# Kernel optimization log

Hardware: AMD Instinct MI355X
Metric: run time of the kernel (lower is better)

The kernel has to match this reference:

```python
import jax, jax.numpy as jnp
import numpy as np

N_PATHS = 200000
PATH_LEN = 8
N_LINKS = 20000
MAX_PL = 100  # max paths crossing a link
DIM = 16
ITERS = 8
# min-max normalization constants: (min, scale) as in set_min_max_scores
MM_TRAFFIC = (0.0, 1e-4)
MM_PACKETS = (0.0, 1e-2)
MM_PKTSIZE = (0.0, 1e-3)
MM_CAP = (0.0, 1e-1)


def _gru(x, h, k, rk, b):
    # Keras GRUCell, reset_after=True. b: [2, 3*units] (input bias, recurrent bias)
    mx = x @ k + b[0]
    mi = h @ rk + b[1]
    xz, xr, xh = jnp.split(mx, 3, axis=-1)
    rz, rr, rh = jnp.split(mi, 3, axis=-1)
    z = jax.nn.sigmoid(xz + rz)
    r = jax.nn.sigmoid(xr + rr)
    hh = jnp.tanh(xh + r * rh)
    return z * h + (1.0 - z) * hh


def setup_inputs() -> dict:
    key = jax.random.key(0)
    ks = jax.random.split(key, 24)
    f32 = jnp.float32
    inp = {}
    inp['flow_traffic'] = jax.random.uniform(ks[0], (N_PATHS, 1), f32, 100.0, 10000.0)
    inp['flow_packets'] = jax.random.uniform(ks[1], (N_PATHS, 1), f32, 1.0, 100.0)
    inp['flow_packet_size'] = jax.random.uniform(ks[2], (N_PATHS, 1), f32, 100.0, 1500.0)
    inp['flow_type'] = jax.random.uniform(ks[3], (N_PATHS, 2), f32)
    inp['link_capacity'] = jax.random.uniform(ks[4], (N_LINKS, 1), f32, 10.0, 100.0)
    inp['link_to_path'] = jax.random.randint(ks[5], (N_PATHS, PATH_LEN), 0, N_LINKS, jnp.int32)
    p_idx = jax.random.randint(ks[6], (N_LINKS, MAX_PL), 0, N_PATHS, jnp.int32)
    s_idx = jax.random.randint(ks[7], (N_LINKS, MAX_PL), 0, PATH_LEN + 1, jnp.int32)
    inp['path_to_link'] = jnp.stack([p_idx, s_idx], axis=-1)

    def dense(k, i, o):
        return jax.random.normal(k, (i, o), f32) * (1.0 / np.sqrt(i))

    inp['fe_w1'] = dense(ks[8], 5, DIM);   inp['fe_b1'] = jnp.zeros((DIM,), f32)
    inp['fe_w2'] = dense(ks[9], DIM, DIM); inp['fe_b2'] = jnp.zeros((DIM,), f32)
    inp['le_w1'] = dense(ks[10], 2, DIM);  inp['le_b1'] = jnp.zeros((DIM,), f32)
    inp['le_w2'] = dense(ks[11], DIM, DIM); inp['le_b2'] = jnp.zeros((DIM,), f32)
    inp['pgru_k'] = dense(ks[12], DIM, 3 * DIM)
    inp['pgru_rk'] = dense(ks[13], DIM, 3 * DIM)
    inp['pgru_b'] = jnp.zeros((2, 3 * DIM), f32)
    inp['lgru_k'] = dense(ks[14], DIM, 3 * DIM)
    inp['lgru_rk'] = dense(ks[15], DIM, 3 * DIM)
    inp['lgru_b'] = jnp.zeros((2, 3 * DIM), f32)
    inp['ro_w1'] = dense(ks[16], DIM, DIM // 2); inp['ro_b1'] = jnp.zeros((DIM // 2,), f32)
    inp['ro_w2'] = dense(ks[17], DIM // 2, DIM // 4); inp['ro_b2'] = jnp.zeros((DIM // 4,), f32)
    inp['ro_w3'] = dense(ks[18], DIM // 4, 1); inp['ro_b3'] = jnp.zeros((1,), f32)
    return inp


def reference(flow_traffic, flow_packets, flow_packet_size, flow_type, link_capacity,
              link_to_path, path_to_link,
              fe_w1, fe_b1, fe_w2, fe_b2, le_w1, le_b1, le_w2, le_b2,
              pgru_k, pgru_rk, pgru_b, lgru_k, lgru_rk, lgru_b,
              ro_w1, ro_b1, ro_w2, ro_b2, ro_w3, ro_b3):
    relu = jax.nn.relu
    # load per link: sum traffic of crossing paths / capacity
    load = jnp.sum(flow_traffic[path_to_link[:, :, 0]], axis=1) / (link_capacity * 1e9)  # [L,1]

    flow_feats = jnp.concatenate([
        (flow_traffic - MM_TRAFFIC[0]) * MM_TRAFFIC[1],
        (flow_packets - MM_PACKETS[0]) * MM_PACKETS[1],
        (flow_packet_size - MM_PKTSIZE[0]) * MM_PKTSIZE[1],
        flow_type], axis=1)  # [P,5]
    path_state = relu(relu(flow_feats @ fe_w1 + fe_b1) @ fe_w2 + fe_b2)  # [P,16]

    link_feats = jnp.concatenate([(link_capacity - MM_CAP[0]) * MM_CAP[1], load], axis=1)  # [L,2]
    link_state = relu(relu(link_feats @ le_w1 + le_b1) @ le_w2 + le_b2)  # [L,16]

    for _ in range(ITERS):
        link_gather = link_state[link_to_path]  # [P, path_len, 16]
        prev = path_state

        def step(h, x):
            h2 = _gru(x, h, pgru_k, pgru_rk, pgru_b)
            return h2, h2

        path_state, seq = jax.lax.scan(step, prev, jnp.swapaxes(link_gather, 0, 1))
        seq = jnp.swapaxes(seq, 0, 1)  # [P, path_len, 16]
        path_state_sequence = jnp.concatenate([prev[:, None, :], seq], axis=1)  # [P, path_len+1, 16]
        # gather_nd: (path_idx, seq_pos) pairs per link
        path_gather = path_state_sequence[path_to_link[:, :, 0], path_to_link[:, :, 1]]  # [L, MAX_PL, 16]
        path_sum = jnp.sum(path_gather, axis=1)  # [L,16]
        link_state = _gru(path_sum, link_state, lgru_k, lgru_rk, lgru_b)

    h1 = relu(path_state_sequence[:, 1:] @ ro_w1 + ro_b1)
    h2 = relu(h1 @ ro_w2 + ro_b2)
    occupancy = jax.nn.softplus(h2 @ ro_w3 + ro_b3)  # [P, path_len, 1]
    capacity_gather = link_capacity[link_to_path]  # [P, path_len, 1]
    delay = jnp.sum(occupancy / capacity_gather, axis=1)  # [P,1]
    return delay
```

## Files before the change

### kernel.cpp

```cpp
#include <hip/hip_runtime.h>
#include <hip/hip_bf16.h>
#include <math.h>

#define N_PATHS  200000
#define PATH_LEN 8
#define N_LINKS  20000
#define MAX_PL   100
#define DIM      16
#define ITERS    8

typedef __attribute__((ext_vector_type(8))) short bf16x8;
typedef __attribute__((ext_vector_type(4))) float f32x4;

#define SEQ_BYTES  64000000ull
#define LS_BYTES   1280000ull
#define LREC_BYTES 1280000ull
#define P2L_BYTES  8000000ull
#define SLOT_BYTES 6400000u

__device__ __forceinline__ float fast_sigmoid(float x) {
    return __builtin_amdgcn_rcpf(1.0f + __expf(-x));
}
__device__ __forceinline__ float fast_tanh(float x) {
    float ax = fabsf(x);
    float t  = __expf(-2.0f * ax);
    float r  = (1.0f - t) * __builtin_amdgcn_rcpf(1.0f + t);
    return copysignf(r, x);
}
__device__ __forceinline__ float softplusf_(float x) {
    return fmaxf(x, 0.0f) + log1pf(expf(-fabsf(x)));
}
__device__ __forceinline__ float bflo(unsigned int u) {
    union { unsigned int i; float f; } c; c.i = u << 16; return c.f;
}
__device__ __forceinline__ float bfhi(unsigned int u) {
    union { unsigned int i; float f; } c; c.i = u & 0xffff0000u; return c.f;
}
__device__ __forceinline__ unsigned int pk_bf16(float lo, float hi) {
    unsigned int r;
    asm("v_cvt_pk_bf16_f32 %0, %1, %2" : "=v"(r) : "v"(lo), "v"(hi));
    return r;
}
__device__ __forceinline__ unsigned short bf16_1(float v) {
    return (unsigned short)(pk_bf16(v, v) & 0xffffu);
}

union U8 { unsigned int u[4]; bf16x8 v; };

__global__ __launch_bounds__(256) void k_pack(const int* __restrict__ p2l,
                                              unsigned int* __restrict__ outE,
                                              unsigned int* __restrict__ outO)
{
    int i = blockIdx.x * 256 + threadIdx.x;
    if (i < N_LINKS * MAX_PL) {
        unsigned int pi = (unsigned int)p2l[2 * i];
        unsigned int si = (unsigned int)p2l[2 * i + 1];
        unsigned int sE = (si == 0) ? 8u : ((si == 8) ? 9u : si);
        unsigned int sO = (si == 0) ? 9u : ((si == 8) ? 8u : si);
        outE[i] = (sE << 18) | pi;
        outO[i] = (sO << 18) | pi;
    }
}

__global__ __launch_bounds__(64) void k_init_links(
    const float* __restrict__ traffic, const float* __restrict__ cap,
    const int* __restrict__ p2l,
    const float* __restrict__ le_w1, const float* __restrict__ le_b1,
    const float* __restrict__ le_w2, const float* __restrict__ le_b2,
    const float* __restrict__ kk, const float* __restrict__ pb,
    float* __restrict__ ls, unsigned short* __restrict__ lrec)
{
    int l = blockIdx.x;
    int lane = threadIdx.x;
    float s = 0.0f;
    for (int j = lane; j < MAX_PL; j += 64) {
        int p = p2l[(size_t)(l * MAX_PL + j) * 2 + 0];
        s += traffic[p];
    }
    #pragma unroll
    for (int off = 32; off > 0; off >>= 1) s += __shfl_xor(s, off);

    float c = cap[l];
    float f0 = c * 0.1f;
    float f1 = s / (c * 1e9f);

    float h1[DIM];
    #pragma unroll
    for (int d = 0; d < DIM; d++)
        h1[d] = fmaxf(f0 * le_w1[d] + f1 * le_w1[DIM + d] + le_b1[d], 0.0f);

    float h2[DIM];
    #pragma unroll
    for (int d = 0; d < DIM; d++) {
        float a = le_b2[d];
        #pragma unroll
        for (int k = 0; k < DIM; k++) a = fmaf(h1[k], le_w2[k * DIM + d], a);
        h2[d] = fmaxf(a, 0.0f);
    }
    if (lane < DIM) ls[(size_t)l * DIM + lane] = h2[lane];
    if (lane < DIM) {
        float mh = pb[32 + lane];
        #pragma unroll
        for (int k = 0; k < DIM; k++) mh = fmaf(h2[k], kk[k * 48 + 32 + lane], mh);
        unsigned short* rec = lrec + (size_t)l * 32;
        int q = lane >> 2, idx = lane & 3;
        rec[q * 8 + idx]     = bf16_1(h2[lane]);
        rec[q * 8 + 4 + idx] = bf16_1(mh);
    }
}

__global__ __launch_bounds__(256) void k_init_paths(
    const float* __restrict__ traffic, const float* __restrict__ packets,
    const float* __restrict__ pktsize, const float* __restrict__ ftype,
    const float* __restrict__ fe_w1, const float* __restrict__ fe_b1,
    const float* __restrict__ fe_w2, const float* __restrict__ fe_b2,
    unsigned short* __restrict__ seq)
{
    int p = blockIdx.x * blockDim.x + threadIdx.x;
    if (p >= N_PATHS) return;
    float f[5];
    f[0] = traffic[p] * 0.0001f;
    f[1] = packets[p] * 0.01f;
    f[2] = pktsize[p] * 0.001f;
    f[3] = ftype[p * 2 + 0];
    f[4] = ftype[p * 2 + 1];

    float h1[DIM];
    #pragma unroll
    for (int d = 0; d < DIM; d++) {
        float a = fe_b1[d];
        #pragma unroll
        for (int k = 0; k < 5; k++) a = fmaf(f[k], fe_w1[k * DIM + d], a);
        h1[d] = fmaxf(a, 0.0f);
    }
    float h2[DIM];
    #pragma unroll
    for (int d = 0; d < DIM; d++) {
        float a = fe_b2[d];
        #pragma unroll
        for (int k = 0; k < DIM; k++) a = fmaf(h1[k], fe_w2[k * DIM + d], a);
        h2[d] = fmaxf(a, 0.0f);
    }
    unsigned int pkd[8];
    #pragma unroll
    for (int q = 0; q < 8; q++) pkd[q] = pk_bf16(h2[2 * q], h2[2 * q + 1]);
    uint4* out = (uint4*)(seq + ((size_t)8 * N_PATHS + p) * DIM);
    out[0] = make_uint4(pkd[0], pkd[1], pkd[2], pkd[3]);
    out[1] = make_uint4(pkd[4], pkd[5], pkd[6], pkd[7]);
}

__global__ __launch_bounds__(256, 4) void k_paths(
    const int* __restrict__ l2p, const unsigned short* __restrict__ lrec,
    const float* __restrict__ rk, const float* __restrict__ kk,
    const float* __restrict__ b,
    unsigned short* __restrict__ seq, int ps, int cs)
{
    int l = threadIdx.x & 63;
    int wave = (blockIdx.x * 256 + threadIdx.x) >> 6;
    int pr = l & 15;
    int g  = l >> 4;
    int kq = g * 4;
    int p  = wave * 16 + pr;

    U8 Az, Ar, Ah;
    {
        #pragma unroll
        for (int i = 0; i < 2; i++) {
            int k0 = (kq + 2 * i) * 48, k1 = (kq + 2 * i + 1) * 48;
            Az.u[i]     = pk_bf16(rk[k0 + pr],      rk[k1 + pr]);
            Az.u[2 + i] = pk_bf16(kk[k0 + pr],      kk[k1 + pr]);
            Ar.u[i]     = pk_bf16(rk[k0 + 16 + pr], rk[k1 + 16 + pr]);
            Ar.u[2 + i] = pk_bf16(kk[k0 + 16 + pr], kk[k1 + 16 + pr]);
            Ah.u[i]     = pk_bf16(rk[k0 + 32 + pr], rk[k1 + 32 + pr]);
            Ah.u[2 + i] = 0;
        }
    }
    f32x4 Cz, Cr, Ch;
    #pragma unroll
    for (int r = 0; r < 4; r++) {
        Cz[r] = b[kq + r]      + b[48 + kq + r];
        Cr[r] = b[16 + kq + r] + b[64 + kq + r];
        Ch[r] = b[80 + kq + r];
    }

    int4 ia = *(const int4*)(l2p + (size_t)p * 8);
    int4 ib = *(const int4*)(l2p + (size_t)p * 8 + 4);
#define IDX(t) ((t) == 0 ? ia.x : (t) == 1 ? ia.y : (t) == 2 ? ia.z : (t) == 3 ? ia.w : \
                (t) == 4 ? ib.x : (t) == 5 ? ib.y : (t) == 6 ? ib.z : ib.w)

    const char* lrecc = (const char*)lrec;
    char* seqc = (char*)seq;
    unsigned g16 = (unsigned)(g * 16);
    unsigned sbase = (unsigned)p * 32u + (unsigned)(g * 8);
    unsigned csoff = (unsigned)cs * SLOT_BYTES + sbase;

    uint4 X[8];
    #pragma unroll
    for (int t = 0; t < 8; t++)
        X[t] = *(const uint4*)(lrecc + (unsigned)IDX(t) * 64u + g16);

    float h0, h1, h2, h3;
    U8 B;
    {
        uint2 hp = *(const uint2*)(seqc + ((unsigned)ps * SLOT_BYTES + sbase));
        h0 = bflo(hp.x); h1 = bfhi(hp.x); h2 = bflo(hp.y); h3 = bfhi(hp.y);
        B.u[0] = hp.x; B.u[1] = hp.y;
    }

#define STEPX(t, soff) { \
    B.u[2] = X[t].x; B.u[3] = X[t].y; \
    f32x4 az = __builtin_amdgcn_mfma_f32_16x16x32_bf16(Az.v, B.v, Cz, 0, 0, 0); \
    f32x4 ar = __builtin_amdgcn_mfma_f32_16x16x32_bf16(Ar.v, B.v, Cr, 0, 0, 0); \
    f32x4 ah = __builtin_amdgcn_mfma_f32_16x16x32_bf16(Ah.v, B.v, Ch, 0, 0, 0); \
    float z0 = fast_sigmoid(az[0]), z1 = fast_sigmoid(az[1]); \
    float z2 = fast_sigmoid(az[2]), z3 = fast_sigmoid(az[3]); \
    float r0 = fast_sigmoid(ar[0]), r1 = fast_sigmoid(ar[1]); \
    float r2 = fast_sigmoid(ar[2]), r3 = fast_sigmoid(ar[3]); \
    float q0 = fast_tanh(bflo(X[t].z) + r0 * ah[0]); \
    float q1 = fast_tanh(bfhi(X[t].z) + r1 * ah[1]); \
    float q2 = fast_tanh(bflo(X[t].w) + r2 * ah[2]); \
    float q3 = fast_tanh(bfhi(X[t].w) + r3 * ah[3]); \
    h0 = z0 * h0 + (1.0f - z0) * q0; \
    h1 = z1 * h1 + (1.0f - z1) * q1; \
    h2 = z2 * h2 + (1.0f - z2) * q2; \
    h3 = z3 * h3 + (1.0f - z3) * q3; \
    unsigned int p01 = pk_bf16(h0, h1), p23 = pk_bf16(h2, h3); \
    *(uint2*)(seqc + (soff)) = make_uint2(p01, p23); \
    B.u[0] = p01; B.u[1] = p23; }

    STEPX(0, 1u * SLOT_BYTES + sbase)
    STEPX(1, 2u * SLOT_BYTES + sbase)
    STEPX(2, 3u * SLOT_BYTES + sbase)
    STEPX(3, 4u * SLOT_BYTES + sbase)
    STEPX(4, 5u * SLOT_BYTES + sbase)
    STEPX(5, 6u * SLOT_BYTES + sbase)
    STEPX(6, 7u * SLOT_BYTES + sbase)
    STEPX(7, csoff)
#undef STEPX
#undef IDX
}

__global__ __launch_bounds__(256) void k_links(
    const unsigned int* __restrict__ p2lp, const unsigned short* __restrict__ seq,
    const float* __restrict__ lk, const float* __restrict__ lrk,
    const float* __restrict__ lb,
    const float* __restrict__ kk, const float* __restrict__ pb,
    float* ls, unsigned short* __restrict__ lrec)
{
    int lane = threadIdx.x & 63;
    int l = blockIdx.x * 4 + (threadIdx.x >> 6);
    size_t base = (size_t)l * MAX_PL;
    int half = lane & 1;
    int r0 = lane >> 1;

    unsigned int e0 = p2lp[base + r0];
    unsigned int e1 = p2lp[base + r0 + 32];
    unsigned int e2 = p2lp[base + r0 + 64];

    const unsigned short* sh = seq + half * 8;
    unsigned int pi, si;
    pi = e0 & 0x3FFFFu; si = e0 >> 18;
    uint4 a0 = *(const uint4*)(sh + ((size_t)si * N_PATHS + pi) * DIM);
    pi = e1 & 0x3FFFFu; si = e1 >> 18;
    uint4 a1 = *(const uint4*)(sh + ((size_t)si * N_PATHS + pi) * DIM);
    pi = e2 & 0x3FFFFu; si = e2 >> 18;
    uint4 a2 = *(const uint4*)(sh + ((size_t)si * N_PATHS + pi) * DIM);

    float acc[8];
    #pragma unroll
    for (int i = 0; i < 8; i++) acc[i] = 0.0f;
    unsigned int selLo = 0x00003F80u;
    unsigned int selHi = 0x3F800000u;

#define DOTU(u, i0) \
    asm("v_dot2_f32_bf16 %0, %1, %2, %0" : "+v"(acc[i0]) : "v"(u), "v"(selLo)); \
    asm("v_dot2_f32_bf16 %0, %1, %2, %0" : "+v"(acc[i0 + 1]) : "v"(u), "v"(selHi));
#define DOT8(a) DOTU(a.x, 0) DOTU(a.y, 2) DOTU(a.z, 4) DOTU(a.w, 6)

    DOT8(a0) DOT8(a1) DOT8(a2)
    if (r0 < 4) {
        unsigned int e3 = p2lp[base + r0 + 96];
        pi = e3 & 0x3FFFFu; si = e3 >> 18;
        uint4 a3 = *(const uint4*)(sh + ((size_t)si * N_PATHS + pi) * DIM);
        DOT8(a3)
    }
#undef DOTU
#undef DOT8

    float v4[4];
    {
        int sel = (lane & 2) ? 4 : 0;
        #pragma unroll
        for (int i = 0; i < 4; i++)
            v4[i] = acc[sel + i] + __shfl_xor(acc[(4 - sel) + i], 2);
    }
    float v2[2];
    {
        int sel = (lane & 4) ? 2 : 0;
        #pragma unroll
        for (int i = 0; i < 2; i++)
            v2[i] = v4[sel + i] + __shfl_xor(v4[(2 - sel) + i], 4);
    }
    float s;
    {
        int sel = (lane & 8) ? 1 : 0;
        s = v2[sel] + __shfl_xor(v2[1 - sel], 8);
    }
    s += __shfl_xor(s, 16);
    s += __shfl_xor(s, 32);

    float accf[16];
    #pragma unroll
    for (int k = 0; k < 16; k++) {
        int src = ((k >> 3) & 1) | (((k >> 2) & 1) << 1) | (((k >> 1) & 1) << 2) | ((k & 1) << 3);
        accf[k] = __shfl(s, src);
    }

    float h[DIM];
    #pragma unroll
    for (int d = 0; d < DIM; d++) h[d] = ls[(size_t)l * DIM + d];

    int j = (lane < 48) ? lane : 0;
    float mx = lb[j];
    float mi = lb[48 + j];
    #pragma unroll
    for (int k = 0; k < DIM; k++) {
        mx = fmaf(accf[k], lk[k * 48 + j], mx);
        mi = fmaf(h[k],   lrk[k * 48 + j], mi);
    }

    int d = lane & 15;
    float xz = __shfl(mx, d),      rz = __shfl(mi, d);
    float xr = __shfl(mx, d + 16), rr = __shfl(mi, d + 16);
    float xh = __shfl(mx, d + 32), rh = __shfl(mi, d + 32);
    float z  = fast_sigmoid(xz + rz);
    float r  = fast_sigmoid(xr + rr);
    float hh = fast_tanh(xh + r * rh);
    float hn = z * h[d] + (1.0f - z) * hh;

    if (lane < DIM) ls[(size_t)l * DIM + lane] = hn;

    float hf[DIM];
    #pragma unroll
    for (int k = 0; k < DIM; k++) hf[k] = __shfl(hn, k);
    if (lane < DIM) {
        float mh = pb[32 + lane];
        #pragma unroll
        for (int k = 0; k < DIM; k++) mh = fmaf(hf[k], kk[k * 48 + 32 + lane], mh);
        unsigned short* rec = lrec + (size_t)l * 32;
        int q = lane >> 2, idx = lane & 3;
        rec[q * 8 + idx]     = bf16_1(hn);
        rec[q * 8 + 4 + idx] = bf16_1(mh);
    }
}

__global__ __launch_bounds__(256) void k_readout(
    const unsigned short* __restrict__ seq, const int* __restrict__ l2p,
    const float* __restrict__ cap,
    const float* __restrict__ w1, const float* __restrict__ b1,
    const float* __restrict__ w2, const float* __restrict__ b2,
    const float* __restrict__ w3, const float* __restrict__ b3,
    float* __restrict__ out)
{
    int p = blockIdx.x * blockDim.x + threadIdx.x;
    if (p >= N_PATHS) return;
    float delay = 0.0f;
    for (int t = 1; t <= PATH_LEN; t++) {
        const uint4* gp = (const uint4*)(seq + ((size_t)t * N_PATHS + p) * DIM);
        uint4 a = gp[0], c = gp[1];
        float h[DIM];
        h[0]  = bflo(a.x); h[1]  = bfhi(a.x); h[2]  = bflo(a.y); h[3]  = bfhi(a.y);
        h[4]  = bflo(a.z); h[5]  = bfhi(a.z); h[6]  = bflo(a.w); h[7]  = bfhi(a.w);
        h[8]  = bflo(c.x); h[9]  = bfhi(c.x); h[10] = bflo(c.y); h[11] = bfhi(c.y);
        h[12] = bflo(c.z); h[13] = bfhi(c.z); h[14] = bflo(c.w); h[15] = bfhi(c.w);

        float h1[8];
        #pragma unroll
        for (int jj = 0; jj < 8; jj++) {
            float a1 = b1[jj];
            #pragma unroll
            for (int k = 0; k < DIM; k++) a1 = fmaf(h[k], w1[k * 8 + jj], a1);
            h1[jj] = fmaxf(a1, 0.0f);
        }
        float h2[4];
        #pragma unroll
        for (int jj = 0; jj < 4; jj++) {
            float a2 = b2[jj];
            #pragma unroll
            for (int k = 0; k < 8; k++) a2 = fmaf(h1[k], w2[k * 4 + jj], a2);
            h2[jj] = fmaxf(a2, 0.0f);
        }
        float o = b3[0];
        #pragma unroll
        for (int k = 0; k < 4; k++) o = fmaf(h2[k], w3[k], o);
        o = softplusf_(o);

        float cp = cap[l2p[(size_t)p * PATH_LEN + (t - 1)]];
        delay += o / cp;
    }
    out[p] = delay;
}

extern "C" void kernel_launch(void* const* d_in, const int* in_sizes, int n_in,
                              void* d_out, int out_size, void* d_ws, size_t ws_size,
                              hipStream_t stream)
{
    const float* flow_traffic = (const float*)d_in[0];
    const float* flow_packets = (const float*)d_in[1];
    const float* flow_pktsize = (const float*)d_in[2];
    const float* flow_type    = (const float*)d_in[3];
    const float* link_cap     = (const float*)d_in[4];
    const int*   l2p          = (const int*)d_in[5];
    const int*   p2l          = (const int*)d_in[6];
    const float* fe_w1 = (const float*)d_in[7];
    const float* fe_b1 = (const float*)d_in[8];
    const float* fe_w2 = (const float*)d_in[9];
    const float* fe_b2 = (const float*)d_in[10];
    const float* le_w1 = (const float*)d_in[11];
    const float* le_b1 = (const float*)d_in[12];
    const float* le_w2 = (const float*)d_in[13];
    const float* le_b2 = (const float*)d_in[14];
    const float* pgru_k  = (const float*)d_in[15];
    const float* pgru_rk = (const float*)d_in[16];
    const float* pgru_b  = (const float*)d_in[17];
    const float* lgru_k  = (const float*)d_in[18];
    const float* lgru_rk = (const float*)d_in[19];
    const float* lgru_b  = (const float*)d_in[20];
    const float* ro_w1 = (const float*)d_in[21];
    const float* ro_b1 = (const float*)d_in[22];
    const float* ro_w2 = (const float*)d_in[23];
    const float* ro_b2 = (const float*)d_in[24];
    const float* ro_w3 = (const float*)d_in[25];
    const float* ro_b3 = (const float*)d_in[26];
    float* out = (float*)d_out;

    char* ws = (char*)d_ws;
    unsigned short* seq   = (unsigned short*)ws;
    float*          ls    = (float*)(ws + SEQ_BYTES);
    unsigned short* lrec  = (unsigned short*)(ws + SEQ_BYTES + LS_BYTES);
    unsigned int*   p2lpE = (unsigned int*)(ws + SEQ_BYTES + LS_BYTES + LREC_BYTES);
    unsigned int*   p2lpO = (unsigned int*)(ws + SEQ_BYTES + LS_BYTES + LREC_BYTES + P2L_BYTES);

    k_pack<<<(N_LINKS * MAX_PL + 255) / 256, 256, 0, stream>>>(p2l, p2lpE, p2lpO);
    k_init_links<<<N_LINKS, 64, 0, stream>>>(flow_traffic, link_cap, p2l,
        le_w1, le_b1, le_w2, le_b2, pgru_k, pgru_b, ls, lrec);
    k_init_paths<<<(N_PATHS + 255) / 256, 256, 0, stream>>>(flow_traffic,
        flow_packets, flow_pktsize, flow_type, fe_w1, fe_b1, fe_w2, fe_b2, seq);

    for (int it = 0; it < ITERS; ++it) {
        int ps = (it & 1) ? 9 : 8;
        int cs = (it & 1) ? 8 : 9;
        k_paths<<<(N_PATHS / 16) / 4, 256, 0, stream>>>(l2p, lrec, pgru_rk,
            pgru_k, pgru_b, seq, ps, cs);
        if (it != ITERS - 1)
            k_links<<<N_LINKS / 4, 256, 0, stream>>>((it & 1) ? p2lpO : p2lpE,
                seq, lgru_k, lgru_rk, lgru_b, pgru_k, pgru_b, ls, lrec);
    }

    k_readout<<<(N_PATHS + 255) / 256, 256, 0, stream>>>(seq, l2p, link_cap,
        ro_w1, ro_b1, ro_w2, ro_b2, ro_w3, ro_b3, out);
}
```

Before: 561.2 us.

## Fuse readout MLP into final path GRU pass and drop separate readout kernel

The last path-GRU iteration becomes a dedicated kernel that runs the readout MLP right after each step. The first layer uses an MFMA and the rest runs in registers with a cross-lane shuffle, so the final sequence states are never written to or re-read from global memory. Softplus switches to hardware exp2/log approximations, and the occupancy hint on k_paths is dropped. This removes one kernel launch and the readout's pass over the sequence buffer, at the cost of more registers in the fused kernel and a bf16 first readout layer.

```diff
diff --git a/kernel.cpp b/kernel.cpp
--- a/kernel.cpp
+++ b/kernel.cpp
@@ -27,8 +27,10 @@
     float r  = (1.0f - t) * __builtin_amdgcn_rcpf(1.0f + t);
     return copysignf(r, x);
 }
-__device__ __forceinline__ float softplusf_(float x) {
-    return fmaxf(x, 0.0f) + log1pf(expf(-fabsf(x)));
+__device__ __forceinline__ float fast_softplus(float x) {
+    float e = __builtin_amdgcn_exp2f(-fabsf(x) * 1.44269504f);
+    float lg = __builtin_amdgcn_logf(1.0f + e);
+    return fmaxf(x, 0.0f) + 0.69314718f * lg;
 }
 __device__ __forceinline__ float bflo(unsigned int u) {
     union { unsigned int i; float f; } c; c.i = u << 16; return c.f;
@@ -149,7 +151,7 @@
     out[1] = make_uint4(pkd[4], pkd[5], pkd[6], pkd[7]);
 }
 
-__global__ __launch_bounds__(256, 4) void k_paths(
+__global__ __launch_bounds__(256) void k_paths(
     const int* __restrict__ l2p, const unsigned short* __restrict__ lrec,
     const float* __restrict__ rk, const float* __restrict__ kk,
     const float* __restrict__ b,
@@ -237,7 +239,136 @@
     STEPX(6, 7u * SLOT_BYTES + sbase)
     STEPX(7, csoff)
 #undef STEPX
+}
+
+__global__ __launch_bounds__(256) void k_paths_last(
+    const int* __restrict__ l2p, const unsigned short* __restrict__ lrec,
+    const float* __restrict__ rk, const float* __restrict__ kk,
+    const float* __restrict__ b,
+    const unsigned short* __restrict__ seq,
+    const float* __restrict__ cap,
+    const float* __restrict__ w1, const float* __restrict__ b1,
+    const float* __restrict__ w2, const float* __restrict__ b2,
+    const float* __restrict__ w3, const float* __restrict__ b3,
+    float* __restrict__ out, int ps)
+{
+    int l = threadIdx.x & 63;
+    int wave = (blockIdx.x * 256 + threadIdx.x) >> 6;
+    int pr = l & 15;
+    int g  = l >> 4;
+    int kq = g * 4;
+    int p  = wave * 16 + pr;
+
+    U8 Az, Ar, Ah, A1;
+    {
+        #pragma unroll
+        for (int i = 0; i < 2; i++) {
+            int k0 = (kq + 2 * i) * 48, k1 = (kq + 2 * i + 1) * 48;
+            Az.u[i]     = pk_bf16(rk[k0 + pr],      rk[k1 + pr]);
+            Az.u[2 + i] = pk_bf16(kk[k0 + pr],      kk[k1 + pr]);
+            Ar.u[i]     = pk_bf16(rk[k0 + 16 + pr], rk[k1 + 16 + pr]);
+            Ar.u[2 + i] = pk_bf16(kk[k0 + 16 + pr], kk[k1 + 16 + pr]);
+            Ah.u[i]     = pk_bf16(rk[k0 + 32 + pr], rk[k1 + 32 + pr]);
+            Ah.u[2 + i] = 0;
+            A1.u[i]     = (pr < 8) ? pk_bf16(w1[(kq + 2 * i) * 8 + pr],
+                                             w1[(kq + 2 * i + 1) * 8 + pr]) : 0u;
+            A1.u[2 + i] = 0;
+        }
+    }
+    f32x4 Cz, Cr, Ch, C1;
+    #pragma unroll
+    for (int r = 0; r < 4; r++) {
+        Cz[r] = b[kq + r]      + b[48 + kq + r];
+        Cr[r] = b[16 + kq + r] + b[64 + kq + r];
+        Ch[r] = b[80 + kq + r];
+        C1[r] = (kq + r < 8) ? b1[kq + r] : 0.0f;
+    }
+    float W2[8][4], B2v[4], W3[4], B3v;
+    #pragma unroll
+    for (int k = 0; k < 8; k++)
+        #pragma unroll
+        for (int j = 0; j < 4; j++) W2[k][j] = w2[k * 4 + j];
+    #pragma unroll
+    for (int j = 0; j < 4; j++) B2v[j] = b2[j];
+    #pragma unroll
+    for (int j = 0; j < 4; j++) W3[j] = w3[j];
+    B3v = b3[0];
+
+    int4 ia = *(const int4*)(l2p + (size_t)p * 8);
+    int4 ib = *(const int4*)(l2p + (size_t)p * 8 + 4);
+
+    const char* lrecc = (const char*)lrec;
+    const char* seqc = (const char*)seq;
+    unsigned g16 = (unsigned)(g * 16);
+    unsigned sbase = (unsigned)p * 32u + (unsigned)(g * 8);
+
+    uint4 X[8];
+    float capv[8];
+    #pragma unroll
+    for (int t = 0; t < 8; t++) {
+        int li = IDX(t);
+        X[t] = *(const uint4*)(lrecc + (unsigned)li * 64u + g16);
+        capv[t] = cap[li];
+    }
+
+    float h0, h1, h2, h3;
+    U8 B;
+    {
+        uint2 hp = *(const uint2*)(seqc + ((unsigned)ps * SLOT_BYTES + sbase));
+        h0 = bflo(hp.x); h1 = bfhi(hp.x); h2 = bflo(hp.y); h3 = bfhi(hp.y);
+        B.u[0] = hp.x; B.u[1] = hp.y;
+    }
+    U8 Bro;
+    Bro.u[2] = 0; Bro.u[3] = 0;
+    float delay = 0.0f;
+
+#define STEPL(t) { \
+    B.u[2] = X[t].x; B.u[3] = X[t].y; \
+    f32x4 az = __builtin_amdgcn_mfma_f32_16x16x32_bf16(Az.v, B.v, Cz, 0, 0, 0); \
+    f32x4 ar = __builtin_amdgcn_mfma_f32_16x16x32_bf16(Ar.v, B.v, Cr, 0, 0, 0); \
+    f32x4 ah = __builtin_amdgcn_mfma_f32_16x16x32_bf16(Ah.v, B.v, Ch, 0, 0, 0); \
+    float z0 = fast_sigmoid(az[0]), z1 = fast_sigmoid(az[1]); \
+    float z2 = fast_sigmoid(az[2]), z3 = fast_sigmoid(az[3]); \
+    float r0 = fast_sigmoid(ar[0]), r1 = fast_sigmoid(ar[1]); \
+    float r2 = fast_sigmoid(ar[2]), r3 = fast_sigmoid(ar[3]); \
+    float q0 = fast_tanh(bflo(X[t].z) + r0 * ah[0]); \
+    float q1 = fast_tanh(bfhi(X[t].z) + r1 * ah[1]); \
+    float q2 = fast_tanh(bflo(X[t].w) + r2 * ah[2]); \
+    float q3 = fast_tanh(bfhi(X[t].w) + r3 * ah[3]); \
+    h0 = z0 * h0 + (1.0f - z0) * q0; \
+    h1 = z1 * h1 + (1.0f - z1) * q1; \
+    h2 = z2 * h2 + (1.0f - z2) * q2; \
+    h3 = z3 * h3 + (1.0f - z3) * q3; \
+    unsigned int p01 = pk_bf16(h0, h1), p23 = pk_bf16(h2, h3); \
+    B.u[0] = p01; B.u[1] = p23; \
+    Bro.u[0] = p01; Bro.u[1] = p23; \
+    f32x4 d1 = __builtin_amdgcn_mfma_f32_16x16x32_bf16(A1.v, Bro.v, C1, 0, 0, 0); \
+    float e0 = fmaxf(d1[0], 0.0f), e1 = fmaxf(d1[1], 0.0f); \
+    float e2 = fmaxf(d1[2], 0.0f), e3 = fmaxf(d1[3], 0.0f); \
+    float f0 = __shfl_xor(e0, 16), f1 = __shfl_xor(e1, 16); \
+    float f2 = __shfl_xor(e2, 16), f3 = __shfl_xor(e3, 16); \
+    float hh2[4]; \
+    _Pragma("unroll") \
+    for (int j = 0; j < 4; j++) { \
+        float a2 = B2v[j]; \
+        a2 = fmaf(e0, W2[0][j], a2); a2 = fmaf(e1, W2[1][j], a2); \
+        a2 = fmaf(e2, W2[2][j], a2); a2 = fmaf(e3, W2[3][j], a2); \
+        a2 = fmaf(f0, W2[4][j], a2); a2 = fmaf(f1, W2[5][j], a2); \
+        a2 = fmaf(f2, W2[6][j], a2); a2 = fmaf(f3, W2[7][j], a2); \
+        hh2[j] = fmaxf(a2, 0.0f); \
+    } \
+    float o = B3v; \
+    o = fmaf(hh2[0], W3[0], o); o = fmaf(hh2[1], W3[1], o); \
+    o = fmaf(hh2[2], W3[2], o); o = fmaf(hh2[3], W3[3], o); \
+    o = fast_softplus(o); \
+    delay += o * __builtin_amdgcn_rcpf(capv[t]); }
+
+    STEPL(0) STEPL(1) STEPL(2) STEPL(3)
+    STEPL(4) STEPL(5) STEPL(6) STEPL(7)
+#undef STEPL
 #undef IDX
+
+    if (g == 0) out[p] = delay;
 }
 
 __global__ __launch_bounds__(256) void k_links(
@@ -352,53 +483,6 @@
         rec[q * 8 + idx]     = bf16_1(hn);
         rec[q * 8 + 4 + idx] = bf16_1(mh);
     }
-}
-
-__global__ __launch_bounds__(256) void k_readout(
-    const unsigned short* __restrict__ seq, const int* __restrict__ l2p,
-    const float* __restrict__ cap,
-    const float* __restrict__ w1, const float* __restrict__ b1,
-    const float* __restrict__ w2, const float* __restrict__ b2,
-    const float* __restrict__ w3, const float* __restrict__ b3,
-    float* __restrict__ out)
-{
-    int p = blockIdx.x * blockDim.x + threadIdx.x;
-    if (p >= N_PATHS) return;
-    float delay = 0.0f;
-    for (int t = 1; t <= PATH_LEN; t++) {
-        const uint4* gp = (const uint4*)(seq + ((size_t)t * N_PATHS + p) * DIM);
-        uint4 a = gp[0], c = gp[1];
-        float h[DIM];
-        h[0]  = bflo(a.x); h[1]  = bfhi(a.x); h[2]  = bflo(a.y); h[3]  = bfhi(a.y);
-        h[4]  = bflo(a.z); h[5]  = bfhi(a.z); h[6]  = bflo(a.w); h[7]  = bfhi(a.w);
-        h[8]  = bflo(c.x); h[9]  = bfhi(c.x); h[10] = bflo(c.y); h[11] = bfhi(c.y);
-        h[12] = bflo(c.z); h[13] = bfhi(c.z); h[14] = bflo(c.w); h[15] = bfhi(c.w);
-
-        float h1[8];
-        #pragma unroll
-        for (int jj = 0; jj < 8; jj++) {
-            float a1 = b1[jj];
-            #pragma unroll
-            for (int k = 0; k < DIM; k++) a1 = fmaf(h[k], w1[k * 8 + jj], a1);
-            h1[jj] = fmaxf(a1, 0.0f);
-        }
-        float h2[4];
-        #pragma unroll
-        for (int jj = 0; jj < 4; jj++) {
-            float a2 = b2[jj];
-            #pragma unroll
-            for (int k = 0; k < 8; k++) a2 = fmaf(h1[k], w2[k * 4 + jj], a2);
-            h2[jj] = fmaxf(a2, 0.0f);
-        }
-        float o = b3[0];
-        #pragma unroll
-        for (int k = 0; k < 4; k++) o = fmaf(h2[k], w3[k], o);
-        o = softplusf_(o);
-
-        float cp = cap[l2p[(size_t)p * PATH_LEN + (t - 1)]];
-        delay += o / cp;
-    }
-    out[p] = delay;
 }
 
 extern "C" void kernel_launch(void* const* d_in, const int* in_sizes, int n_in,
@@ -447,16 +531,15 @@
     k_init_paths<<<(N_PATHS + 255) / 256, 256, 0, stream>>>(flow_traffic,
         flow_packets, flow_pktsize, flow_type, fe_w1, fe_b1, fe_w2, fe_b2, seq);
 
-    for (int it = 0; it < ITERS; ++it) {
+    for (int it = 0; it < ITERS - 1; ++it) {
         int ps = (it & 1) ? 9 : 8;
         int cs = (it & 1) ? 8 : 9;
         k_paths<<<(N_PATHS / 16) / 4, 256, 0, stream>>>(l2p, lrec, pgru_rk,
             pgru_k, pgru_b, seq, ps, cs);
-        if (it != ITERS - 1)
-            k_links<<<N_LINKS / 4, 256, 0, stream>>>((it & 1) ? p2lpO : p2lpE,
-                seq, lgru_k, lgru_rk, lgru_b, pgru_k, pgru_b, ls, lrec);
-    }
-
-    k_readout<<<(N_PATHS + 255) / 256, 256, 0, stream>>>(seq, l2p, link_cap,
-        ro_w1, ro_b1, ro_w2, ro_b2, ro_w3, ro_b3, out);
-}
+        k_links<<<N_LINKS / 4, 256, 0, stream>>>((it & 1) ? p2lpO : p2lpE,
+            seq, lgru_k, lgru_rk, lgru_b, pgru_k, pgru_b, ls, lrec);
+    }
+    k_paths_last<<<(N_PATHS / 16) / 4, 256, 0, stream>>>(l2p, lrec, pgru_rk,
+        pgru_k, pgru_b, seq, link_cap,
+        ro_w1, ro_b1, ro_w2, ro_b2, ro_w3, ro_b3, out, 9);
+}
```

After: 561.5 us. About the same (+0.0%).
